# Kernel optimization log

Measured on AMD Instinct MI355X. Metric: run time of the kernel, lower is better.

The kernel has to match this reference:

```python
import jax, jax.numpy as jnp
import numpy as np


def setup_inputs() -> dict:
    key = jax.random.key(0)
    k1, k2, k3 = jax.random.split(key, 3)
    B, C, H, W = 64, 512, 28, 28
    K = 32
    std = 1.0 / (K * C) ** 0.5
    x = jax.random.normal(k1, (B, C, H, W), dtype=jnp.float32)
    codewords = jax.random.uniform(k2, (K, C), dtype=jnp.float32, minval=-std, maxval=std)
    scale = jax.random.uniform(k3, (K,), dtype=jnp.float32, minval=-1.0, maxval=0.0)
    return {"x": x, "codewords": codewords, "scale": scale}


def reference(x, codewords, scale):
    # x: (B, C, H, W) -> descriptors (B, N, C)
    B, C, H, W = x.shape
    K = codewords.shape[0]
    xd = x.reshape(B, C, H * W).transpose(0, 2, 1)  # (B, N, C)

    # scaled L2: scale_k * ||x_n - c_k||^2, expanded without (B,N,K,C) intermediate
    x_sq = jnp.sum(xd * xd, axis=-1, keepdims=True)            # (B, N, 1)
    c_sq = jnp.sum(codewords * codewords, axis=-1)             # (K,)
    xc = jnp.einsum("bnc,kc->bnk", xd, codewords)              # (B, N, K)
    dist = scale * (x_sq - 2.0 * xc + c_sq)                    # (B, N, K)

    A = jax.nn.softmax(dist, axis=2)                           # (B, N, K)

    # encoded_k = sum_n A[b,n,k] * (x[b,n] - c[k])
    wx = jnp.einsum("bnk,bnc->bkc", A, xd)                     # (B, K, C)
    wsum = jnp.sum(A, axis=1)                                  # (B, K)
    encoded = wx - wsum[:, :, None] * codewords[None, :, :]    # (B, K, C)
    return encoded
```

## Files before the change

### kernel.cpp

```cpp
#include <hip/hip_runtime.h>
#include <hip/hip_bf16.h>

#define BB 64
#define CC 512
#define NPIX 784
#define KK 32

typedef __attribute__((ext_vector_type(8))) short short8;
typedef __attribute__((ext_vector_type(4))) float floatx4;
typedef __attribute__((ext_vector_type(4))) unsigned short ushort4v;


__device__ __forceinline__ unsigned short f2bf(float f) {
    union { float f; unsigned u; } v; v.f = f;
    return (unsigned short)((v.u + 0x7FFFu + ((v.u >> 16) & 1u)) >> 16);
}
__device__ __forceinline__ float bf2f(unsigned short h) {
    union { unsigned u; float f; } v; v.u = ((unsigned)h) << 16; return v.f;
}

#define CW_S 520
#define AT_S 72

__global__ __launch_bounds__(256) void k1(const float* __restrict__ x,
                                          const float* __restrict__ cw,
                                          const float* __restrict__ scale,
                                          unsigned short* __restrict__ At)
{
    __shared__ unsigned short cs[KK * CW_S];
    __shared__ unsigned short At_l[KK * AT_S];
    __shared__ float xsq_l[4][16];
    __shared__ float csq_p[8][KK];
    __shared__ float csq_l[KK];

    const int t    = threadIdx.x;
    const int lane = t & 63;
    const int w    = t >> 6;
    const int col  = lane & 15;
    const int quad = lane >> 4;
    const int b    = blockIdx.y;
    const int px0  = blockIdx.x * 64;

#pragma unroll 4
    for (int j = 0; j < 16; ++j) {
        const int qidx = t + j * 256;
        const int row = qidx >> 7;
        const int qc  = qidx & 127;
        const float4 v = *(const float4*)&cw[row * CC + qc * 4];
        ushort4v p; p.x = f2bf(v.x); p.y = f2bf(v.y); p.z = f2bf(v.z); p.w = f2bf(v.w);
        *(ushort4v*)&cs[row * CW_S + qc * 4] = p;
    }
    __syncthreads();
    {
        const int k = t & 31, part = t >> 5;
        float s = 0.f;
        for (int i = 0; i < 64; ++i) {
            const float v = bf2f(cs[k * CW_S + part * 64 + i]);
            s += v * v;
        }
        csq_p[part][k] = s;
    }
    __syncthreads();
    if (t < KK) {
        float s = 0.f;
#pragma unroll
        for (int p = 0; p < 8; ++p) s += csq_p[p][t];
        csq_l[t] = s;
    }

    int px = px0 + w * 16 + col;
    if (px > NPIX - 1) px = NPIX - 1;
    const float* xb = x + (size_t)b * CC * NPIX + px;

    floatx4 acc0 = {0.f, 0.f, 0.f, 0.f};
    floatx4 acc1 = {0.f, 0.f, 0.f, 0.f};
    float xsqp = 0.f;

#pragma unroll 4
    for (int kc = 0; kc < 16; ++kc) {
        const int cb = kc * 32 + quad * 8;
        float v[8];
#pragma unroll
        for (int j = 0; j < 8; ++j) v[j] = xb[(size_t)(cb + j) * NPIX];
#pragma unroll
        for (int j = 0; j < 8; ++j) xsqp += v[j] * v[j];
        short8 a;
#pragma unroll
        for (int j = 0; j < 8; ++j) a[j] = (short)f2bf(v[j]);
        const short8 b0 = *(const short8*)&cs[col * CW_S + cb];
        const short8 b1 = *(const short8*)&cs[(col + 16) * CW_S + cb];
        acc0 = __builtin_amdgcn_mfma_f32_16x16x32_bf16(a, b0, acc0, 0, 0, 0);
        acc1 = __builtin_amdgcn_mfma_f32_16x16x32_bf16(a, b1, acc1, 0, 0, 0);
    }

    xsqp += __shfl_xor(xsqp, 16);
    xsqp += __shfl_xor(xsqp, 32);
    if (quad == 0) xsq_l[w][col] = xsqp;
    __syncthreads();

    const float s0 = scale[col], s1 = scale[col + 16];
    const float q0 = csq_l[col], q1 = csq_l[col + 16];
#pragma unroll
    for (int r = 0; r < 4; ++r) {
        const float xq = xsq_l[w][quad * 4 + r];
        const float d0 = s0 * (xq + q0 - 2.f * acc0[r]);
        const float d1 = s1 * (xq + q1 - 2.f * acc1[r]);
        float mx = fmaxf(d0, d1);
        mx = fmaxf(mx, __shfl_xor(mx, 1));
        mx = fmaxf(mx, __shfl_xor(mx, 2));
        mx = fmaxf(mx, __shfl_xor(mx, 4));
        mx = fmaxf(mx, __shfl_xor(mx, 8));
        const float e0 = __expf(d0 - mx), e1 = __expf(d1 - mx);
        float sm = e0 + e1;
        sm += __shfl_xor(sm, 1);
        sm += __shfl_xor(sm, 2);
        sm += __shfl_xor(sm, 4);
        sm += __shfl_xor(sm, 8);
        const float inv = 1.f / sm;
        const int pxl = w * 16 + quad * 4 + r;
        At_l[col * AT_S + pxl]        = f2bf(e0 * inv);
        At_l[(col + 16) * AT_S + pxl] = f2bf(e1 * inv);
    }
    __syncthreads();

    {
        const int k = t >> 3, oct = t & 7;
        if (px0 + oct * 8 + 7 < NPIX) {
            const short8 v = *(const short8*)&At_l[k * AT_S + oct * 8];
            *(short8*)&At[((size_t)b * KK + k) * NPIX + px0 + oct * 8] = v;
        }
    }
}

#define K2_PT 160
#define K2_S  168

__global__ __launch_bounds__(256) void k2(const float* __restrict__ x,
                                          const float* __restrict__ cw,
                                          const unsigned short* __restrict__ At,
                                          float* __restrict__ out)
{
    __shared__ unsigned short xs[64 * K2_S];
    __shared__ unsigned short as[KK * K2_S];
    __shared__ float wsum_l[KK];

    const int t    = threadIdx.x;
    const int lane = t & 63;
    const int w    = t >> 6;
    const int col  = lane & 15;
    const int quad = lane >> 4;
    const int b    = blockIdx.y;
    const int c0   = blockIdx.x * 64;

    const float* xb = x + (size_t)b * CC * NPIX;
    const unsigned short* ab = At + (size_t)b * KK * NPIX;

    floatx4 acc0 = {0.f, 0.f, 0.f, 0.f};
    floatx4 acc1 = {0.f, 0.f, 0.f, 0.f};
    float wacc[8];
#pragma unroll
    for (int i = 0; i < 8; ++i) wacc[i] = 0.f;

    for (int ch = 0; ch < 5; ++ch) {
        const int pt0 = ch * K2_PT;
        __syncthreads();
#pragma unroll 2
        for (int j = 0; j < 10; ++j) {
            const int qidx = t + j * 256;
            const int cr = qidx / 40, pq = qidx - cr * 40;
            const int gpx = pt0 + pq * 4;
            ushort4v p;
            if (gpx < NPIX) {
                const float4 v = *(const float4*)&xb[(size_t)(c0 + cr) * NPIX + gpx];
                p.x = f2bf(v.x); p.y = f2bf(v.y); p.z = f2bf(v.z); p.w = f2bf(v.w);
            } else { p.x = 0; p.y = 0; p.z = 0; p.w = 0; }
            *(ushort4v*)&xs[cr * K2_S + pq * 4] = p;
        }
#pragma unroll
        for (int j = 0; j < 5; ++j) {
            const int qidx = t + j * 256;
            const int k = qidx / 40, pq = qidx - k * 40;
            const int gpx = pt0 + pq * 4;
            ushort4v p;
            if (gpx < NPIX) p = *(const ushort4v*)&ab[(size_t)k * NPIX + gpx];
            else { p.x = 0; p.y = 0; p.z = 0; p.w = 0; }
            *(ushort4v*)&as[k * K2_S + pq * 4] = p;
        }
        __syncthreads();

#pragma unroll
        for (int kk = 0; kk < 8; ++kk) {
            const int k = w * 8 + kk;
            float v = bf2f(as[k * K2_S + lane]) + bf2f(as[k * K2_S + 64 + lane]);
            const float v3 = bf2f(as[k * K2_S + 128 + (lane & 31)]);
            wacc[kk] += v + ((lane < 32) ? v3 : 0.f);
        }

#pragma unroll
        for (int s = 0; s < 5; ++s) {
            const int off = s * 32 + quad * 8;
            const short8 av0 = *(const short8*)&as[col * K2_S + off];
            const short8 av1 = *(const short8*)&as[(col + 16) * K2_S + off];
            const short8 bv  = *(const short8*)&xs[(w * 16 + col) * K2_S + off];
            acc0 = __builtin_amdgcn_mfma_f32_16x16x32_bf16(av0, bv, acc0, 0, 0, 0);
            acc1 = __builtin_amdgcn_mfma_f32_16x16x32_bf16(av1, bv, acc1, 0, 0, 0);
        }
    }

#pragma unroll
    for (int kk = 0; kk < 8; ++kk) {
        float v = wacc[kk];
        v += __shfl_xor(v, 1);  v += __shfl_xor(v, 2);  v += __shfl_xor(v, 4);
        v += __shfl_xor(v, 8);  v += __shfl_xor(v, 16); v += __shfl_xor(v, 32);
        if (lane == 0) wsum_l[w * 8 + kk] = v;
    }
    __syncthreads();

    const int c = c0 + w * 16 + col;
#pragma unroll
    for (int r = 0; r < 4; ++r) {
        const int ka = quad * 4 + r, kb = ka + 16;
        out[((size_t)b * KK + ka) * CC + c] = acc0[r] - wsum_l[ka] * cw[ka * CC + c];
        out[((size_t)b * KK + kb) * CC + c] = acc1[r] - wsum_l[kb] * cw[kb * CC + c];
    }
}

extern "C" void kernel_launch(void* const* d_in, const int* in_sizes, int n_in,
                              void* d_out, int out_size, void* d_ws, size_t ws_size,
                              hipStream_t stream) {
    const float* x     = (const float*)d_in[0];
    const float* cw    = (const float*)d_in[1];
    const float* scale = (const float*)d_in[2];
    float* out = (float*)d_out;
    unsigned short* At = (unsigned short*)d_ws;

    k1<<<dim3(13, BB), dim3(256), 0, stream>>>(x, cw, scale, At);
    k2<<<dim3(CC / 64, BB), dim3(256), 0, stream>>>(x, cw, At, out);
}
```

Before: 195.0 us.

## Fuse assignment and aggregation per pixel split, reduce partials in separate kernel

Merges the softmax-assignment and weighted-aggregation kernels into one kernel that handles a 112-pixel slice per block. The block keeps A in shared memory and reuses it against x tiles loaded from the same slice, so the bf16 A round trip through global memory goes away and the second kernel no longer streams x from scratch. Partial (K,C) sums and weight sums for each of 7 splits go to workspace, and a small third kernel reduces them and subtracts the codeword term. The cost is extra workspace traffic (7x B*K*C floats written and read) and a grid of only 448 blocks. The first-stage loads are also software-pipelined with double buffering.

```diff
diff --git a/kernel.cpp b/kernel.cpp
--- a/kernel.cpp
+++ b/kernel.cpp
@@ -5,11 +5,17 @@
 #define CC 512
 #define NPIX 784
 #define KK 32
+#define NSPL 7
+#define PXB 112
+#define CW_S 520
+#define XA_S 136
 
 typedef __attribute__((ext_vector_type(8))) short short8;
 typedef __attribute__((ext_vector_type(4))) float floatx4;
 typedef __attribute__((ext_vector_type(4))) unsigned short ushort4v;
 
+#define OFF_WP 0
+#define OFF_WS (NSPL*BB*KK*CC)
 
 __device__ __forceinline__ unsigned short f2bf(float f) {
     union { float f; unsigned u; } v; v.f = f;
@@ -19,33 +25,33 @@
     union { unsigned u; float f; } v; v.u = ((unsigned)h) << 16; return v.f;
 }
 
-#define CW_S 520
-#define AT_S 72
-
-__global__ __launch_bounds__(256) void k1(const float* __restrict__ x,
-                                          const float* __restrict__ cw,
-                                          const float* __restrict__ scale,
-                                          unsigned short* __restrict__ At)
+__global__ __launch_bounds__(256) void k_fused(const float* __restrict__ x,
+                                               const float* __restrict__ cw,
+                                               const float* __restrict__ scale,
+                                               float* __restrict__ ws)
 {
-    __shared__ unsigned short cs[KK * CW_S];
-    __shared__ unsigned short At_l[KK * AT_S];
-    __shared__ float xsq_l[4][16];
+    __shared__ __align__(16) unsigned char u8[128 * XA_S * 2];
+    __shared__ __align__(16) unsigned short A_l[KK * XA_S];
     __shared__ float csq_p[8][KK];
     __shared__ float csq_l[KK];
-
-    const int t    = threadIdx.x;
-    const int lane = t & 63;
-    const int w    = t >> 6;
-    const int col  = lane & 15;
-    const int quad = lane >> 4;
-    const int b    = blockIdx.y;
-    const int px0  = blockIdx.x * 64;
+    __shared__ float wred[KK][8];
+
+    unsigned short* cs = (unsigned short*)u8;
+    unsigned short* xs = (unsigned short*)u8;
+
+    const int t     = threadIdx.x;
+    const int lane  = t & 63;
+    const int w     = t >> 6;
+    const int col   = lane & 15;
+    const int quad  = lane >> 4;
+    const int split = blockIdx.x;
+    const int b     = blockIdx.y;
+    const int p0    = split * PXB;
 
 #pragma unroll 4
     for (int j = 0; j < 16; ++j) {
         const int qidx = t + j * 256;
-        const int row = qidx >> 7;
-        const int qc  = qidx & 127;
+        const int row = qidx >> 7, qc = qidx & 127;
         const float4 v = *(const float4*)&cw[row * CC + qc * 4];
         ushort4v p; p.x = f2bf(v.x); p.y = f2bf(v.y); p.z = f2bf(v.z); p.w = f2bf(v.w);
         *(ushort4v*)&cs[row * CW_S + qc * 4] = p;
@@ -67,162 +73,183 @@
         for (int p = 0; p < 8; ++p) s += csq_p[p][t];
         csq_l[t] = s;
     }
-
-    int px = px0 + w * 16 + col;
-    if (px > NPIX - 1) px = NPIX - 1;
-    const float* xb = x + (size_t)b * CC * NPIX + px;
-
-    floatx4 acc0 = {0.f, 0.f, 0.f, 0.f};
-    floatx4 acc1 = {0.f, 0.f, 0.f, 0.f};
-    float xsqp = 0.f;
-
-#pragma unroll 4
-    for (int kc = 0; kc < 16; ++kc) {
-        const int cb = kc * 32 + quad * 8;
-        float v[8];
-#pragma unroll
-        for (int j = 0; j < 8; ++j) v[j] = xb[(size_t)(cb + j) * NPIX];
-#pragma unroll
-        for (int j = 0; j < 8; ++j) xsqp += v[j] * v[j];
-        short8 a;
-#pragma unroll
-        for (int j = 0; j < 8; ++j) a[j] = (short)f2bf(v[j]);
-        const short8 b0 = *(const short8*)&cs[col * CW_S + cb];
-        const short8 b1 = *(const short8*)&cs[(col + 16) * CW_S + cb];
-        acc0 = __builtin_amdgcn_mfma_f32_16x16x32_bf16(a, b0, acc0, 0, 0, 0);
-        acc1 = __builtin_amdgcn_mfma_f32_16x16x32_bf16(a, b1, acc1, 0, 0, 0);
-    }
-
-    xsqp += __shfl_xor(xsqp, 16);
-    xsqp += __shfl_xor(xsqp, 32);
-    if (quad == 0) xsq_l[w][col] = xsqp;
     __syncthreads();
 
     const float s0 = scale[col], s1 = scale[col + 16];
     const float q0 = csq_l[col], q1 = csq_l[col + 16];
-#pragma unroll
-    for (int r = 0; r < 4; ++r) {
-        const float xq = xsq_l[w][quad * 4 + r];
-        const float d0 = s0 * (xq + q0 - 2.f * acc0[r]);
-        const float d1 = s1 * (xq + q1 - 2.f * acc1[r]);
-        float mx = fmaxf(d0, d1);
-        mx = fmaxf(mx, __shfl_xor(mx, 1));
-        mx = fmaxf(mx, __shfl_xor(mx, 2));
-        mx = fmaxf(mx, __shfl_xor(mx, 4));
-        mx = fmaxf(mx, __shfl_xor(mx, 8));
-        const float e0 = __expf(d0 - mx), e1 = __expf(d1 - mx);
-        float sm = e0 + e1;
-        sm += __shfl_xor(sm, 1);
-        sm += __shfl_xor(sm, 2);
-        sm += __shfl_xor(sm, 4);
-        sm += __shfl_xor(sm, 8);
-        const float inv = 1.f / sm;
-        const int pxl = w * 16 + quad * 4 + r;
-        At_l[col * AT_S + pxl]        = f2bf(e0 * inv);
-        At_l[(col + 16) * AT_S + pxl] = f2bf(e1 * inv);
+
+    for (int pt = w; pt < NSPL; pt += 4) {
+        const int px = p0 + pt * 16 + col;
+        const float* xb = x + (size_t)b * CC * NPIX + px;
+
+        floatx4 acc0 = {0.f, 0.f, 0.f, 0.f};
+        floatx4 acc1 = {0.f, 0.f, 0.f, 0.f};
+        float xsqp = 0.f;
+        float va[8], vb[8];
+
+#pragma unroll
+        for (int j = 0; j < 8; ++j) va[j] = xb[(size_t)(quad * 8 + j) * NPIX];
+
+#pragma unroll
+        for (int kc = 0; kc < 16; kc += 2) {
+            {
+                const int cb = (kc + 1) * 32 + quad * 8;
+#pragma unroll
+                for (int j = 0; j < 8; ++j) vb[j] = xb[(size_t)(cb + j) * NPIX];
+            }
+            {
+#pragma unroll
+                for (int j = 0; j < 8; ++j) xsqp += va[j] * va[j];
+                short8 a;
+#pragma unroll
+                for (int j = 0; j < 8; ++j) a[j] = (short)f2bf(va[j]);
+                const int cb0 = kc * 32 + quad * 8;
+                const short8 b0 = *(const short8*)&cs[col * CW_S + cb0];
+                const short8 b1 = *(const short8*)&cs[(col + 16) * CW_S + cb0];
+                acc0 = __builtin_amdgcn_mfma_f32_16x16x32_bf16(a, b0, acc0, 0, 0, 0);
+                acc1 = __builtin_amdgcn_mfma_f32_16x16x32_bf16(a, b1, acc1, 0, 0, 0);
+            }
+            if (kc + 2 < 16) {
+                const int cb = (kc + 2) * 32 + quad * 8;
+#pragma unroll
+                for (int j = 0; j < 8; ++j) va[j] = xb[(size_t)(cb + j) * NPIX];
+            }
+            {
+#pragma unroll
+                for (int j = 0; j < 8; ++j) xsqp += vb[j] * vb[j];
+                short8 a;
+#pragma unroll
+                for (int j = 0; j < 8; ++j) a[j] = (short)f2bf(vb[j]);
+                const int cb1 = (kc + 1) * 32 + quad * 8;
+                const short8 b0 = *(const short8*)&cs[col * CW_S + cb1];
+                const short8 b1 = *(const short8*)&cs[(col + 16) * CW_S + cb1];
+                acc0 = __builtin_amdgcn_mfma_f32_16x16x32_bf16(a, b0, acc0, 0, 0, 0);
+                acc1 = __builtin_amdgcn_mfma_f32_16x16x32_bf16(a, b1, acc1, 0, 0, 0);
+            }
+        }
+
+        xsqp += __shfl_xor(xsqp, 16);
+        xsqp += __shfl_xor(xsqp, 32);
+
+#pragma unroll
+        for (int r = 0; r < 4; ++r) {
+            const float xq = __shfl(xsqp, quad * 4 + r);
+            const float d0 = s0 * (xq + q0 - 2.f * acc0[r]);
+            const float d1 = s1 * (xq + q1 - 2.f * acc1[r]);
+            float mx = fmaxf(d0, d1);
+            mx = fmaxf(mx, __shfl_xor(mx, 1));
+            mx = fmaxf(mx, __shfl_xor(mx, 2));
+            mx = fmaxf(mx, __shfl_xor(mx, 4));
+            mx = fmaxf(mx, __shfl_xor(mx, 8));
+            const float e0 = __expf(d0 - mx), e1 = __expf(d1 - mx);
+            float sm = e0 + e1;
+            sm += __shfl_xor(sm, 1);
+            sm += __shfl_xor(sm, 2);
+            sm += __shfl_xor(sm, 4);
+            sm += __shfl_xor(sm, 8);
+            const float inv = 1.f / sm;
+            const int pxl = pt * 16 + quad * 4 + r;
+            A_l[col * XA_S + pxl]        = f2bf(e0 * inv);
+            A_l[(col + 16) * XA_S + pxl] = f2bf(e1 * inv);
+        }
     }
     __syncthreads();
 
     {
-        const int k = t >> 3, oct = t & 7;
-        if (px0 + oct * 8 + 7 < NPIX) {
-            const short8 v = *(const short8*)&At_l[k * AT_S + oct * 8];
-            *(short8*)&At[((size_t)b * KK + k) * NPIX + px0 + oct * 8] = v;
-        }
-    }
-}
-
-#define K2_PT 160
-#define K2_S  168
-
-__global__ __launch_bounds__(256) void k2(const float* __restrict__ x,
-                                          const float* __restrict__ cw,
-                                          const unsigned short* __restrict__ At,
+        const int k = t >> 3, part = t & 7;
+        float s = 0.f;
+#pragma unroll 7
+        for (int i = 0; i < 14; ++i) s += bf2f(A_l[k * XA_S + part * 14 + i]);
+        wred[k][part] = s;
+    }
+    {
+        const ushort4v z = {0, 0, 0, 0};
+        if (t < 128) *(ushort4v*)&A_l[(t >> 2) * XA_S + PXB + (t & 3) * 4] = z;
+#pragma unroll
+        for (int jj = 0; jj < 2; ++jj) {
+            const int q = t + jj * 256;
+            *(ushort4v*)&xs[(q >> 2) * XA_S + PXB + (q & 3) * 4] = z;
+        }
+    }
+    __syncthreads();
+
+    if (t < KK) {
+        float s = 0.f;
+#pragma unroll
+        for (int p = 0; p < 8; ++p) s += wred[t][p];
+        ws[OFF_WS + (size_t)(split * BB + b) * KK + t] = s;
+    }
+
+    const float* xbase = x + (size_t)b * CC * NPIX + p0;
+    float* Wp = ws + OFF_WP;
+
+    for (int cch = 0; cch < 4; ++cch) {
+#pragma unroll 2
+        for (int j = 0; j < 14; ++j) {
+            const int q = t + j * 256;
+            const int row = q / 28, pq = q - row * 28;
+            const float4 v = *(const float4*)&xbase[(size_t)(cch * 128 + row) * NPIX + pq * 4];
+            ushort4v p; p.x = f2bf(v.x); p.y = f2bf(v.y); p.z = f2bf(v.z); p.w = f2bf(v.w);
+            *(ushort4v*)&xs[row * XA_S + pq * 4] = p;
+        }
+        __syncthreads();
+
+        floatx4 a00 = {0.f,0.f,0.f,0.f}, a01 = {0.f,0.f,0.f,0.f};
+        floatx4 a10 = {0.f,0.f,0.f,0.f}, a11 = {0.f,0.f,0.f,0.f};
+#pragma unroll
+        for (int ks = 0; ks < 4; ++ks) {
+            const int off = ks * 32 + quad * 8;
+            const short8 av0 = *(const short8*)&A_l[col * XA_S + off];
+            const short8 av1 = *(const short8*)&A_l[(col + 16) * XA_S + off];
+            const short8 bv0 = *(const short8*)&xs[(w * 32 + col) * XA_S + off];
+            const short8 bv1 = *(const short8*)&xs[(w * 32 + 16 + col) * XA_S + off];
+            a00 = __builtin_amdgcn_mfma_f32_16x16x32_bf16(av0, bv0, a00, 0, 0, 0);
+            a10 = __builtin_amdgcn_mfma_f32_16x16x32_bf16(av1, bv0, a10, 0, 0, 0);
+            a01 = __builtin_amdgcn_mfma_f32_16x16x32_bf16(av0, bv1, a01, 0, 0, 0);
+            a11 = __builtin_amdgcn_mfma_f32_16x16x32_bf16(av1, bv1, a11, 0, 0, 0);
+        }
+
+        const size_t sb = (size_t)(split * BB + b) * KK;
+        const int cb = cch * 128 + w * 32;
+#pragma unroll
+        for (int r = 0; r < 4; ++r) {
+            const int k0 = quad * 4 + r;
+            Wp[(sb + k0) * CC + cb + col]           = a00[r];
+            Wp[(sb + k0) * CC + cb + 16 + col]      = a01[r];
+            Wp[(sb + k0 + 16) * CC + cb + col]      = a10[r];
+            Wp[(sb + k0 + 16) * CC + cb + 16 + col] = a11[r];
+        }
+        __syncthreads();
+    }
+}
+
+__global__ __launch_bounds__(256) void k3(const float* __restrict__ cw,
+                                          const float* __restrict__ ws,
                                           float* __restrict__ out)
 {
-    __shared__ unsigned short xs[64 * K2_S];
-    __shared__ unsigned short as[KK * K2_S];
-    __shared__ float wsum_l[KK];
-
-    const int t    = threadIdx.x;
-    const int lane = t & 63;
-    const int w    = t >> 6;
-    const int col  = lane & 15;
-    const int quad = lane >> 4;
-    const int b    = blockIdx.y;
-    const int c0   = blockIdx.x * 64;
-
-    const float* xb = x + (size_t)b * CC * NPIX;
-    const unsigned short* ab = At + (size_t)b * KK * NPIX;
-
-    floatx4 acc0 = {0.f, 0.f, 0.f, 0.f};
-    floatx4 acc1 = {0.f, 0.f, 0.f, 0.f};
-    float wacc[8];
-#pragma unroll
-    for (int i = 0; i < 8; ++i) wacc[i] = 0.f;
-
-    for (int ch = 0; ch < 5; ++ch) {
-        const int pt0 = ch * K2_PT;
-        __syncthreads();
-#pragma unroll 2
-        for (int j = 0; j < 10; ++j) {
-            const int qidx = t + j * 256;
-            const int cr = qidx / 40, pq = qidx - cr * 40;
-            const int gpx = pt0 + pq * 4;
-            ushort4v p;
-            if (gpx < NPIX) {
-                const float4 v = *(const float4*)&xb[(size_t)(c0 + cr) * NPIX + gpx];
-                p.x = f2bf(v.x); p.y = f2bf(v.y); p.z = f2bf(v.z); p.w = f2bf(v.w);
-            } else { p.x = 0; p.y = 0; p.z = 0; p.w = 0; }
-            *(ushort4v*)&xs[cr * K2_S + pq * 4] = p;
-        }
-#pragma unroll
-        for (int j = 0; j < 5; ++j) {
-            const int qidx = t + j * 256;
-            const int k = qidx / 40, pq = qidx - k * 40;
-            const int gpx = pt0 + pq * 4;
-            ushort4v p;
-            if (gpx < NPIX) p = *(const ushort4v*)&ab[(size_t)k * NPIX + gpx];
-            else { p.x = 0; p.y = 0; p.z = 0; p.w = 0; }
-            *(ushort4v*)&as[k * K2_S + pq * 4] = p;
-        }
-        __syncthreads();
-
-#pragma unroll
-        for (int kk = 0; kk < 8; ++kk) {
-            const int k = w * 8 + kk;
-            float v = bf2f(as[k * K2_S + lane]) + bf2f(as[k * K2_S + 64 + lane]);
-            const float v3 = bf2f(as[k * K2_S + 128 + (lane & 31)]);
-            wacc[kk] += v + ((lane < 32) ? v3 : 0.f);
-        }
-
-#pragma unroll
-        for (int s = 0; s < 5; ++s) {
-            const int off = s * 32 + quad * 8;
-            const short8 av0 = *(const short8*)&as[col * K2_S + off];
-            const short8 av1 = *(const short8*)&as[(col + 16) * K2_S + off];
-            const short8 bv  = *(const short8*)&xs[(w * 16 + col) * K2_S + off];
-            acc0 = __builtin_amdgcn_mfma_f32_16x16x32_bf16(av0, bv, acc0, 0, 0, 0);
-            acc1 = __builtin_amdgcn_mfma_f32_16x16x32_bf16(av1, bv, acc1, 0, 0, 0);
-        }
-    }
-
-#pragma unroll
-    for (int kk = 0; kk < 8; ++kk) {
-        float v = wacc[kk];
-        v += __shfl_xor(v, 1);  v += __shfl_xor(v, 2);  v += __shfl_xor(v, 4);
-        v += __shfl_xor(v, 8);  v += __shfl_xor(v, 16); v += __shfl_xor(v, 32);
-        if (lane == 0) wsum_l[w * 8 + kk] = v;
-    }
-    __syncthreads();
-
-    const int c = c0 + w * 16 + col;
-#pragma unroll
-    for (int r = 0; r < 4; ++r) {
-        const int ka = quad * 4 + r, kb = ka + 16;
-        out[((size_t)b * KK + ka) * CC + c] = acc0[r] - wsum_l[ka] * cw[ka * CC + c];
-        out[((size_t)b * KK + kb) * CC + c] = acc1[r] - wsum_l[kb] * cw[kb * CC + c];
-    }
+    const int idx = blockIdx.x * 256 + threadIdx.x;
+    const int c4 = idx & 127;
+    const int k  = (idx >> 7) & 31;
+    const int b  = idx >> 12;
+
+    const float* Wp = ws + OFF_WP;
+    float4 s = make_float4(0.f, 0.f, 0.f, 0.f);
+#pragma unroll
+    for (int sp = 0; sp < NSPL; ++sp) {
+        const float4 v = *(const float4*)&Wp[((size_t)(sp * BB + b) * KK + k) * CC + c4 * 4];
+        s.x += v.x; s.y += v.y; s.z += v.z; s.w += v.w;
+    }
+    float wsum = 0.f;
+#pragma unroll
+    for (int sp = 0; sp < NSPL; ++sp) wsum += ws[OFF_WS + (size_t)(sp * BB + b) * KK + k];
+
+    const float4 c4f = *(const float4*)&cw[k * CC + c4 * 4];
+    float4 o;
+    o.x = s.x - wsum * c4f.x;
+    o.y = s.y - wsum * c4f.y;
+    o.z = s.z - wsum * c4f.z;
+    o.w = s.w - wsum * c4f.w;
+    *(float4*)&out[(size_t)idx * 4] = o;
 }
 
 extern "C" void kernel_launch(void* const* d_in, const int* in_sizes, int n_in,
@@ -232,8 +259,8 @@
     const float* cw    = (const float*)d_in[1];
     const float* scale = (const float*)d_in[2];
     float* out = (float*)d_out;
-    unsigned short* At = (unsigned short*)d_ws;
-
-    k1<<<dim3(13, BB), dim3(256), 0, stream>>>(x, cw, scale, At);
-    k2<<<dim3(CC / 64, BB), dim3(256), 0, stream>>>(x, cw, At, out);
-}
+    float* ws  = (float*)d_ws;
+
+    k_fused<<<dim3(NSPL, BB), dim3(256), 0, stream>>>(x, cw, scale, ws);
+    k3<<<dim3(BB * KK * CC / 4 / 256), dim3(256), 0, stream>>>(cw, ws, out);
+}
```

New measurement: 185.4 us. 1.05x faster.
